# Optimization experiments

Measured on AMD Instinct MI355X. Metric: run time of the kernel, lower is better.

The kernel has to match this reference:

```python
import jax, jax.numpy as jnp
import numpy as np

D = 100  # hard-coded model dim from the source
L, BS = 4096, 64


def setup_inputs() -> dict:
    key = jax.random.key(0)
    k_x, k_w, k_b, k_s = jax.random.split(key, 4)
    x = jax.random.normal(k_x, (L, BS, 1, D), dtype=jnp.float32)
    # nn.Linear(D, D): weight [D, D] (out, in), bias [D]
    lim = 1.0 / np.sqrt(D)
    W = jax.random.uniform(k_w, (D, D), dtype=jnp.float32, minval=-lim, maxval=lim)
    b = jax.random.uniform(k_b, (D,), dtype=jnp.float32, minval=-lim, maxval=lim)
    # self.states ~ Normal(0, 0.02), shape [D, D]
    states = 0.02 * jax.random.normal(k_s, (D, D), dtype=jnp.float32)
    return {"x": x, "W": W, "b": b, "states": states}


def reference(x, W, b, states):
    # z1 = layer1(x): x [L, BS, 1, D] @ W.T + b
    z1 = jnp.einsum("lbod,ed->lboe", x, W) + b
    # scan: carry = tile(states) is constant across steps (f multiplies by 1.0),
    # so output[i] = z1[i] @ states for every timestep -> one fused batched matmul.
    out = jnp.einsum("lbod,de->lboe", z1, states)
    return out
```

## Files before the change

kernel.cpp:

```cpp
#include <hip/hip_runtime.h>

typedef __bf16 bf16x8 __attribute__((ext_vector_type(8)));
typedef float  f32x4  __attribute__((ext_vector_type(4)));

#define D100 100
#define NROWS (4096*64)
#define NTILES (NROWS/16)
#define NCT 7
#define NKS 4
#define FRAG_ELEMS (NCT*NKS*64*8)
#define TILE_B 6400
#define NBLK (NTILES/8)

typedef const __attribute__((address_space(1))) void gvoid;
typedef __attribute__((address_space(3))) void lvoid;

__global__ __launch_bounds__(256) void prep_kernel(
    const float* __restrict__ W, const float* __restrict__ bvec,
    const float* __restrict__ S, __bf16* __restrict__ wsM) {
  int tid = blockIdx.x * 256 + threadIdx.x;
  if (tid >= FRAG_ELEMS) return;
  int j    = tid & 7;
  int lane = (tid >> 3) & 63;
  int ks   = (tid >> 9) & 3;
  int ct   = tid >> 11;
  int k = ks * 32 + ((lane >> 4) * 8) + j;
  int n = ct * 16 + (lane & 15);
  float acc = 0.f;
  if (n < D100) {
    if (k < D100) {
      float a0 = 0.f, a1 = 0.f, a2 = 0.f, a3 = 0.f;
      for (int d = 0; d < D100; d += 4) {
        a0 += W[(d + 0) * D100 + k] * S[(d + 0) * D100 + n];
        a1 += W[(d + 1) * D100 + k] * S[(d + 1) * D100 + n];
        a2 += W[(d + 2) * D100 + k] * S[(d + 2) * D100 + n];
        a3 += W[(d + 3) * D100 + k] * S[(d + 3) * D100 + n];
      }
      acc = (a0 + a1) + (a2 + a3);
    } else if (k == 112) {
      for (int d = 0; d < D100; ++d) acc += bvec[d] * S[d * D100 + n];
    }
  }
  wsM[tid] = (__bf16)acc;
}

__global__ __launch_bounds__(512, 4) void gemm_kernel(
    const float* __restrict__ x, const __bf16* __restrict__ wsM,
    float* __restrict__ out) {
  __shared__ __align__(16) __bf16 ldsB[FRAG_ELEMS];
  __shared__ __align__(16) float  ldsX[8 * 1600];

  const int t    = threadIdx.x;
  const int lane = t & 63;
  const int l16  = lane & 15;
  const int lg   = lane >> 4;
  const int w    = t >> 6;
  const int tile = blockIdx.x * 8 + w;

  const char* xsrc = (const char*)x + (size_t)tile * TILE_B + (size_t)lane * 16;
  char* ldsx = (char*)(ldsX + w * 1600);
#pragma unroll
  for (int c = 0; c < 6; ++c)
    __builtin_amdgcn_global_load_lds((gvoid*)(xsrc + c * 1024),
                                     (lvoid*)(ldsx + c * 1024), 16, 0, 0);
  if (lane < 16)
    __builtin_amdgcn_global_load_lds((gvoid*)(xsrc + 6144),
                                     (lvoid*)(ldsx + 6144), 16, 0, 0);

  {
    const char* bsrc = (const char*)wsM + (size_t)lane * 16;
    for (int c = w; c < 28; c += 8)
      __builtin_amdgcn_global_load_lds((gvoid*)(bsrc + c * 1024),
                                       (lvoid*)((char*)ldsB + c * 1024),
                                       16, 0, 0);
  }
  __syncthreads();

  f32x4 acc[NCT];
#pragma unroll
  for (int ct = 0; ct < NCT; ++ct) acc[ct] = (f32x4){0.f, 0.f, 0.f, 0.f};

  const bf16x8* Bv = (const bf16x8*)ldsB;
  const char* xrow = ldsx + l16 * 400;

#pragma unroll
  for (int ks = 0; ks < NKS; ++ks) {
    bf16x8 xf;
    if (ks < 3) {
      f32x4 v0 = *(const f32x4*)(xrow + ks * 128 + lg * 32);
      f32x4 v1 = *(const f32x4*)(xrow + ks * 128 + lg * 32 + 16);
#pragma unroll
      for (int j = 0; j < 4; ++j) {
        xf[j]     = (__bf16)v0[j];
        xf[j + 4] = (__bf16)v1[j];
      }
    } else {
      f32x4 v0 = (lg == 0) ? *(const f32x4*)(xrow + 384)
                           : (f32x4){0.f, 0.f, 0.f, 0.f};
#pragma unroll
      for (int j = 0; j < 4; ++j) {
        xf[j]     = (__bf16)v0[j];
        xf[j + 4] = (__bf16)0.f;
      }
      if (lg == 2) xf[0] = (__bf16)1.0f;
    }
#pragma unroll
    for (int ct = 0; ct < NCT; ++ct)
      acc[ct] = __builtin_amdgcn_mfma_f32_16x16x32_bf16(
          Bv[(ct * NKS + ks) * 64 + lane], xf, acc[ct], 0, 0, 0);
  }

#pragma unroll
  for (int ct = 0; ct < NCT; ++ct) {
    if (ct < 6 || lg == 0)
      *(f32x4*)(ldsx + l16 * 400 + ct * 64 + lg * 16) = acc[ct];
  }

  char* dst = (char*)(out + (size_t)tile * 1600) + (size_t)lane * 16;
#pragma unroll
  for (int c = 0; c < 6; ++c) {
    f32x4 v = *(const f32x4*)(ldsx + c * 1024 + lane * 16);
    *(f32x4*)(dst + c * 1024) = v;
  }
  if (lane < 16) {
    f32x4 v = *(const f32x4*)(ldsx + 6144 + lane * 16);
    *(f32x4*)(dst + 6144) = v;
  }
}

extern "C" void kernel_launch(void* const* d_in, const int* in_sizes, int n_in,
                              void* d_out, int out_size, void* d_ws,
                              size_t ws_size, hipStream_t stream) {
  const float* x = (const float*)d_in[0];
  const float* W = (const float*)d_in[1];
  const float* b = (const float*)d_in[2];
  const float* S = (const float*)d_in[3];
  __bf16* wsM = (__bf16*)d_ws;
  float*  out = (float*)d_out;

  hipLaunchKernelGGL(prep_kernel, dim3(56), dim3(256), 0, stream,
                     W, b, S, wsM);
  hipLaunchKernelGGL(gemm_kernel, dim3(NBLK), dim3(512), 0, stream,
                     x, wsM, out);
}
```

Before: 45.18 us.

## Stage x as bf16 in LDS via registers and store output directly

Replaces the async global-to-LDS load of fp32 x tiles with register loads that convert to bf16 before writing to LDS. This halves the LDS footprint per block, and the launch-bounds occupancy hint is raised from 4 to 6. The output epilogue now writes MFMA accumulators straight to global memory instead of staging through LDS for coalesced rows. The aim is less LDS traffic and more resident blocks to hide memory latency, at the cost of less coalesced global stores and extra register pressure.

```diff
diff --git a/kernel.cpp b/kernel.cpp
--- a/kernel.cpp
+++ b/kernel.cpp
@@ -1,6 +1,7 @@
 #include <hip/hip_runtime.h>
 
 typedef __bf16 bf16x8 __attribute__((ext_vector_type(8)));
+typedef __bf16 bf16x4 __attribute__((ext_vector_type(4)));
 typedef float  f32x4  __attribute__((ext_vector_type(4)));
 
 #define D100 100
@@ -9,7 +10,6 @@
 #define NCT 7
 #define NKS 4
 #define FRAG_ELEMS (NCT*NKS*64*8)
-#define TILE_B 6400
 #define NBLK (NTILES/8)
 
 typedef const __attribute__((address_space(1))) void gvoid;
@@ -44,11 +44,11 @@
   wsM[tid] = (__bf16)acc;
 }
 
-__global__ __launch_bounds__(512, 4) void gemm_kernel(
+__global__ __launch_bounds__(512, 6) void gemm_kernel(
     const float* __restrict__ x, const __bf16* __restrict__ wsM,
     float* __restrict__ out) {
   __shared__ __align__(16) __bf16 ldsB[FRAG_ELEMS];
-  __shared__ __align__(16) float  ldsX[8 * 1600];
+  __shared__ __align__(16) __bf16 ldsX[8 * 1600];
 
   const int t    = threadIdx.x;
   const int lane = t & 63;
@@ -57,15 +57,11 @@
   const int w    = t >> 6;
   const int tile = blockIdx.x * 8 + w;
 
-  const char* xsrc = (const char*)x + (size_t)tile * TILE_B + (size_t)lane * 16;
-  char* ldsx = (char*)(ldsX + w * 1600);
+  const char* xsrc = (const char*)x + (size_t)tile * 6400 + (size_t)lane * 16;
+  f32x4 xv[7];
 #pragma unroll
-  for (int c = 0; c < 6; ++c)
-    __builtin_amdgcn_global_load_lds((gvoid*)(xsrc + c * 1024),
-                                     (lvoid*)(ldsx + c * 1024), 16, 0, 0);
-  if (lane < 16)
-    __builtin_amdgcn_global_load_lds((gvoid*)(xsrc + 6144),
-                                     (lvoid*)(ldsx + 6144), 16, 0, 0);
+  for (int c = 0; c < 6; ++c) xv[c] = *(const f32x4*)(xsrc + c * 1024);
+  if (lane < 16) xv[6] = *(const f32x4*)(xsrc + 6144);
 
   {
     const char* bsrc = (const char*)wsM + (size_t)lane * 16;
@@ -74,32 +70,46 @@
                                        (lvoid*)((char*)ldsB + c * 1024),
                                        16, 0, 0);
   }
+
+  __bf16* ldsx = ldsX + w * 1600;
+#pragma unroll
+  for (int c = 0; c < 6; ++c) {
+    bf16x4 h;
+#pragma unroll
+    for (int j = 0; j < 4; ++j) h[j] = (__bf16)xv[c][j];
+    *(bf16x4*)(ldsx + c * 256 + lane * 4) = h;
+  }
+  if (lane < 16) {
+    bf16x4 h;
+#pragma unroll
+    for (int j = 0; j < 4; ++j) h[j] = (__bf16)xv[6][j];
+    *(bf16x4*)(ldsx + 1536 + lane * 4) = h;
+  }
   __syncthreads();
 
   f32x4 acc[NCT];
 #pragma unroll
   for (int ct = 0; ct < NCT; ++ct) acc[ct] = (f32x4){0.f, 0.f, 0.f, 0.f};
 
-  const bf16x8* Bv = (const bf16x8*)ldsB;
-  const char* xrow = ldsx + l16 * 400;
+  const bf16x8* Bv  = (const bf16x8*)ldsB;
+  const __bf16* xrow = ldsx + l16 * D100;
 
 #pragma unroll
   for (int ks = 0; ks < NKS; ++ks) {
     bf16x8 xf;
     if (ks < 3) {
-      f32x4 v0 = *(const f32x4*)(xrow + ks * 128 + lg * 32);
-      f32x4 v1 = *(const f32x4*)(xrow + ks * 128 + lg * 32 + 16);
+      bf16x4 lo = *(const bf16x4*)(xrow + ks * 32 + lg * 8);
+      bf16x4 hi = *(const bf16x4*)(xrow + ks * 32 + lg * 8 + 4);
 #pragma unroll
       for (int j = 0; j < 4; ++j) {
-        xf[j]     = (__bf16)v0[j];
-        xf[j + 4] = (__bf16)v1[j];
+        xf[j]     = lo[j];
+        xf[j + 4] = hi[j];
       }
     } else {
-      f32x4 v0 = (lg == 0) ? *(const f32x4*)(xrow + 384)
-                           : (f32x4){0.f, 0.f, 0.f, 0.f};
+      bf16x4 lo = *(const bf16x4*)(xrow + 96);
 #pragma unroll
       for (int j = 0; j < 4; ++j) {
-        xf[j]     = (__bf16)v0[j];
+        xf[j]     = (lg == 0) ? lo[j] : (__bf16)0.f;
         xf[j + 4] = (__bf16)0.f;
       }
       if (lg == 2) xf[0] = (__bf16)1.0f;
@@ -110,21 +120,11 @@
           Bv[(ct * NKS + ks) * 64 + lane], xf, acc[ct], 0, 0, 0);
   }
 
+  float* orow = out + (size_t)tile * (16 * D100) + l16 * D100 + lg * 4;
 #pragma unroll
   for (int ct = 0; ct < NCT; ++ct) {
     if (ct < 6 || lg == 0)
-      *(f32x4*)(ldsx + l16 * 400 + ct * 64 + lg * 16) = acc[ct];
-  }
-
-  char* dst = (char*)(out + (size_t)tile * 1600) + (size_t)lane * 16;
-#pragma unroll
-  for (int c = 0; c < 6; ++c) {
-    f32x4 v = *(const f32x4*)(ldsx + c * 1024 + lane * 16);
-    *(f32x4*)(dst + c * 1024) = v;
-  }
-  if (lane < 16) {
-    f32x4 v = *(const f32x4*)(ldsx + 6144 + lane * 16);
-    *(f32x4*)(dst + 6144) = v;
+      *(f32x4*)(orow + ct * 16) = acc[ct];
   }
 }
 
```

Measured after the change: 46.91 us. +3.8%, slower.

## Drop LDS staging of fused weights and write outputs directly from registers

Applied to the files above, without the earlier changes.

The GEMM kernel no longer copies the precomputed bf16 weight fragments into shared memory. Each MFMA now reads its B fragment straight from global memory, relying on the cache. The block-wide __syncthreads is replaced by a per-wave vmcnt wait, block size is halved to 4 waves, and results are stored directly from accumulators to global memory instead of being staged through LDS for coalesced writes. This removes LDS traffic and the block barrier and raises occupancy, at the cost of more global/L2 loads for weights and less coalesced, strided output stores.

```diff
diff --git a/kernel.cpp b/kernel.cpp
--- a/kernel.cpp
+++ b/kernel.cpp
@@ -9,8 +9,7 @@
 #define NCT 7
 #define NKS 4
 #define FRAG_ELEMS (NCT*NKS*64*8)
-#define TILE_B 6400
-#define NBLK (NTILES/8)
+#define NBLK (NTILES/4)
 
 typedef const __attribute__((address_space(1))) void gvoid;
 typedef __attribute__((address_space(3))) void lvoid;
@@ -44,20 +43,19 @@
   wsM[tid] = (__bf16)acc;
 }
 
-__global__ __launch_bounds__(512, 4) void gemm_kernel(
+__global__ __launch_bounds__(256, 6) void gemm_kernel(
     const float* __restrict__ x, const __bf16* __restrict__ wsM,
     float* __restrict__ out) {
-  __shared__ __align__(16) __bf16 ldsB[FRAG_ELEMS];
-  __shared__ __align__(16) float  ldsX[8 * 1600];
+  __shared__ __align__(16) float ldsX[4 * 1600];
 
   const int t    = threadIdx.x;
   const int lane = t & 63;
   const int l16  = lane & 15;
   const int lg   = lane >> 4;
   const int w    = t >> 6;
-  const int tile = blockIdx.x * 8 + w;
+  const int tile = blockIdx.x * 4 + w;
 
-  const char* xsrc = (const char*)x + (size_t)tile * TILE_B + (size_t)lane * 16;
+  const char* xsrc = (const char*)x + (size_t)tile * 6400 + (size_t)lane * 16;
   char* ldsx = (char*)(ldsX + w * 1600);
 #pragma unroll
   for (int c = 0; c < 6; ++c)
@@ -67,35 +65,29 @@
     __builtin_amdgcn_global_load_lds((gvoid*)(xsrc + 6144),
                                      (lvoid*)(ldsx + 6144), 16, 0, 0);
 
-  {
-    const char* bsrc = (const char*)wsM + (size_t)lane * 16;
-    for (int c = w; c < 28; c += 8)
-      __builtin_amdgcn_global_load_lds((gvoid*)(bsrc + c * 1024),
-                                       (lvoid*)((char*)ldsB + c * 1024),
-                                       16, 0, 0);
-  }
-  __syncthreads();
+  asm volatile("s_waitcnt vmcnt(0)" ::: "memory");
+  __builtin_amdgcn_sched_barrier(0);
 
   f32x4 acc[NCT];
 #pragma unroll
   for (int ct = 0; ct < NCT; ++ct) acc[ct] = (f32x4){0.f, 0.f, 0.f, 0.f};
 
-  const bf16x8* Bv = (const bf16x8*)ldsB;
-  const char* xrow = ldsx + l16 * 400;
+  const bf16x8* Bv   = (const bf16x8*)wsM;
+  const float*  xrow = (const float*)ldsx + l16 * D100;
 
 #pragma unroll
   for (int ks = 0; ks < NKS; ++ks) {
     bf16x8 xf;
     if (ks < 3) {
-      f32x4 v0 = *(const f32x4*)(xrow + ks * 128 + lg * 32);
-      f32x4 v1 = *(const f32x4*)(xrow + ks * 128 + lg * 32 + 16);
+      f32x4 v0 = *(const f32x4*)(xrow + ks * 32 + lg * 8);
+      f32x4 v1 = *(const f32x4*)(xrow + ks * 32 + lg * 8 + 4);
 #pragma unroll
       for (int j = 0; j < 4; ++j) {
         xf[j]     = (__bf16)v0[j];
         xf[j + 4] = (__bf16)v1[j];
       }
     } else {
-      f32x4 v0 = (lg == 0) ? *(const f32x4*)(xrow + 384)
+      f32x4 v0 = (lg == 0) ? *(const f32x4*)(xrow + 96)
                            : (f32x4){0.f, 0.f, 0.f, 0.f};
 #pragma unroll
       for (int j = 0; j < 4; ++j) {
@@ -105,26 +97,18 @@
       if (lg == 2) xf[0] = (__bf16)1.0f;
     }
 #pragma unroll
-    for (int ct = 0; ct < NCT; ++ct)
-      acc[ct] = __builtin_amdgcn_mfma_f32_16x16x32_bf16(
-          Bv[(ct * NKS + ks) * 64 + lane], xf, acc[ct], 0, 0, 0);
+    for (int ct = 0; ct < NCT; ++ct) {
+      bf16x8 bf = Bv[(ct * NKS + ks) * 64 + lane];
+      acc[ct] = __builtin_amdgcn_mfma_f32_16x16x32_bf16(bf, xf, acc[ct],
+                                                        0, 0, 0);
+    }
   }
 
+  float* orow = out + (size_t)tile * (16 * D100) + l16 * D100 + lg * 4;
 #pragma unroll
   for (int ct = 0; ct < NCT; ++ct) {
     if (ct < 6 || lg == 0)
-      *(f32x4*)(ldsx + l16 * 400 + ct * 64 + lg * 16) = acc[ct];
-  }
-
-  char* dst = (char*)(out + (size_t)tile * 1600) + (size_t)lane * 16;
-#pragma unroll
-  for (int c = 0; c < 6; ++c) {
-    f32x4 v = *(const f32x4*)(ldsx + c * 1024 + lane * 16);
-    *(f32x4*)(dst + c * 1024) = v;
-  }
-  if (lane < 16) {
-    f32x4 v = *(const f32x4*)(ldsx + 6144 + lane * 16);
-    *(f32x4*)(dst + 6144) = v;
+      *(f32x4*)(orow + ct * 16) = acc[ct];
   }
 }
 
@@ -140,6 +124,6 @@
 
   hipLaunchKernelGGL(prep_kernel, dim3(56), dim3(256), 0, stream,
                      W, b, S, wsM);
-  hipLaunchKernelGGL(gemm_kernel, dim3(NBLK), dim3(512), 0, stream,
+  hipLaunchKernelGGL(gemm_kernel, dim3(NBLK), dim3(256), 0, stream,
                      x, wsM, out);
 }
```

After: 58.02 us. +28.4%, slower.
